# Performance work log

Measured on AMD Instinct MI355X. Metric: run time of the kernel, lower is better.

Reference implementation:

```python
import jax, jax.numpy as jnp
import numpy as np

D_MODEL, N_HEADS, D_K, D_V, D_FF, N_LAYERS = 512, 8, 64, 64, 2048, 6
NEG = -1e9
EPS = 1e-5


def layernorm(x):
    # nn.LayerNorm(d_model) created fresh each call: weight=1, bias=0
    mu = jnp.mean(x, axis=-1, keepdims=True)
    var = jnp.var(x, axis=-1, keepdims=True)
    return (x - mu) * jax.lax.rsqrt(var + EPS)


def sinusoidal_pe(seq_len, d_model, dtype=jnp.float32):
    pos = np.arange(seq_len)[:, None].astype(np.float64)
    div = np.exp(np.arange(0, d_model, 2).astype(np.float64) * (-np.log(10000.0) / d_model))
    pe = np.zeros((seq_len, d_model))
    pe[:, 0::2] = np.sin(pos * div)
    pe[:, 1::2] = np.cos(pos * div)
    return jnp.asarray(pe, dtype=dtype)


def mha(q_in, k_in, v_in, mask, Wq, Wk, Wv, Wo):
    # q_in: [B,Lq,D]; k_in/v_in: [B,Lk,D]; mask: [B,Lq,Lk] bool (True = masked)
    B, Lq, _ = q_in.shape
    Lk = k_in.shape[1]
    Q = (q_in @ Wq).reshape(B, Lq, N_HEADS, D_K).transpose(0, 2, 1, 3)
    K = (k_in @ Wk).reshape(B, Lk, N_HEADS, D_K).transpose(0, 2, 1, 3)
    V = (v_in @ Wv).reshape(B, Lk, N_HEADS, D_V).transpose(0, 2, 1, 3)
    scores = jnp.einsum('bhqd,bhkd->bhqk', Q, K) / jnp.sqrt(jnp.asarray(D_K, q_in.dtype))
    scores = jnp.where(mask[:, None, :, :], jnp.asarray(NEG, scores.dtype), scores)
    attn = jax.nn.softmax(scores, axis=-1)
    ctx = jnp.einsum('bhqk,bhkd->bhqd', attn, V)
    ctx = ctx.transpose(0, 2, 1, 3).reshape(B, Lq, N_HEADS * D_V)
    return layernorm(ctx @ Wo + q_in)


def setup_inputs() -> dict:
    key = jax.random.key(0)
    ks = jax.random.split(key, 16)
    B, T, S, V = 8, 1024, 1024, 32000
    s = 0.02
    inp = {
        'dec_inputs': jax.random.randint(ks[0], (B, T), 0, V),
        'enc_inputs': jax.random.randint(ks[1], (B, S), 0, V),
        'enc_outputs': jax.random.normal(ks[2], (B, S, D_MODEL), jnp.float32),
        'emb': jax.random.normal(ks[3], (V, D_MODEL), jnp.float32) * s,
        'Wq_self': jax.random.normal(ks[4], (N_LAYERS, D_MODEL, N_HEADS * D_K), jnp.float32) * s,
        'Wk_self': jax.random.normal(ks[5], (N_LAYERS, D_MODEL, N_HEADS * D_K), jnp.float32) * s,
        'Wv_self': jax.random.normal(ks[6], (N_LAYERS, D_MODEL, N_HEADS * D_V), jnp.float32) * s,
        'Wo_self': jax.random.normal(ks[7], (N_LAYERS, N_HEADS * D_V, D_MODEL), jnp.float32) * s,
        'Wq_cross': jax.random.normal(ks[8], (N_LAYERS, D_MODEL, N_HEADS * D_K), jnp.float32) * s,
        'Wk_cross': jax.random.normal(ks[9], (N_LAYERS, D_MODEL, N_HEADS * D_K), jnp.float32) * s,
        'Wv_cross': jax.random.normal(ks[10], (N_LAYERS, D_MODEL, N_HEADS * D_V), jnp.float32) * s,
        'Wo_cross': jax.random.normal(ks[11], (N_LAYERS, N_HEADS * D_V, D_MODEL), jnp.float32) * s,
        'W1': jax.random.normal(ks[12], (N_LAYERS, D_MODEL, D_FF), jnp.float32) * s,
        'W2': jax.random.normal(ks[13], (N_LAYERS, D_FF, D_MODEL), jnp.float32) * s,
    }
    return inp


def reference(dec_inputs, enc_inputs, enc_outputs, emb, Wq_self, Wk_self, Wv_self, Wo_self,
              Wq_cross, Wk_cross, Wv_cross, Wo_cross, W1, W2):
    B, T = dec_inputs.shape
    S = enc_inputs.shape[1]
    # embedding with padding_idx=0 (row 0 forced to zero)
    emb_eff = emb.at[0].set(0.0)
    x = emb_eff[dec_inputs] + sinusoidal_pe(T, D_MODEL, emb.dtype)[None, :, :]
    # masks: True = masked
    pad_self = (dec_inputs == 0)[:, None, :]                       # [B,1,T]
    causal = jnp.triu(jnp.ones((T, T), bool), k=1)[None, :, :]     # [1,T,T]
    self_mask = pad_self | causal                                  # [B,T,T]
    enc_mask = jnp.broadcast_to((enc_inputs == 0)[:, None, :], (B, T, S))

    def layer(x, p):
        wqs, wks, wvs, wos, wqc, wkc, wvc, woc, w1, w2 = p
        x = mha(x, x, x, self_mask, wqs, wks, wvs, wos)
        x = mha(x, enc_outputs, enc_outputs, enc_mask, wqc, wkc, wvc, woc)
        h = jax.nn.relu(x @ w1) @ w2
        return layernorm(h + x), None

    params = (Wq_self, Wk_self, Wv_self, Wo_self, Wq_cross, Wk_cross, Wv_cross, Wo_cross, W1, W2)
    x, _ = jax.lax.scan(layer, x, params)
    return x
```

## Files before the change

### kernel.cpp

```cpp
#include <hip/hip_runtime.h>
#include <hip/hip_bf16.h>

#define DMODEL 512
#define NH     8
#define DHEAD  64
#define DFF    2048
#define NLAYER 6
#define BB     8
#define TT     1024
#define NTOK   (BB*TT)
#define ACTE   ((size_t)NTOK*DMODEL)

#define QSCALE 0.18033688011112042f

#define RESCALE_THR 8.0f

typedef __bf16  bf16x8  __attribute__((ext_vector_type(8)));
typedef float   float4v __attribute__((ext_vector_type(4)));
typedef short   short4v __attribute__((ext_vector_type(4)));
typedef short   short8v __attribute__((ext_vector_type(8)));

__device__ __forceinline__ unsigned short f2bf(float f) {
    __hip_bfloat16 h = __float2bfloat16(f);
    return *reinterpret_cast<unsigned short*>(&h);
}

__device__ __forceinline__ void gl_lds16(const void* g, void* l) {
    __builtin_amdgcn_global_load_lds((const __attribute__((address_space(1))) void*)g,
                                     (__attribute__((address_space(3))) void*)l, 16, 0, 0);
}

__device__ __forceinline__ int sigma64(int x) {
    return (x & 32) | ((x & 12) << 1) | ((x & 16) >> 2) | (x & 3);
}

struct Tr8Args {
    const float* src[8];
    unsigned short* dst[8];
    int dstL[8];
    int rowOff[8];
};
__global__ __launch_bounds__(256) void transpose8_kernel(Tr8Args a)
{
    __shared__ float tile[64][65];
    const int type = blockIdx.z / 6, lyr = blockIdx.z % 6;
    const float* src = a.src[type] + (size_t)lyr * 512 * 512;
    unsigned short* dst = a.dst[type] + (size_t)lyr * a.dstL[type];
    const int rowOff = a.rowOff[type];
    const int k0 = blockIdx.x * 64, n0 = blockIdx.y * 64;
    const int tid = threadIdx.x;
#pragma unroll
    for (int rep = 0; rep < 16; ++rep) {
        int idx = rep * 256 + tid;
        int r = idx >> 6, c = idx & 63;
        tile[r][c] = src[(size_t)(k0 + r) * 512 + n0 + c];
    }
    __syncthreads();
#pragma unroll
    for (int rep = 0; rep < 16; ++rep) {
        int idx = rep * 256 + tid;
        int r = idx >> 6, c = idx & 63;
        dst[(size_t)(rowOff + n0 + r) * 512 + k0 + c] = f2bf(tile[c][r]);
    }
}

__global__ __launch_bounds__(256) void transpose_conv_kernel(
    const float* __restrict__ W, unsigned short* __restrict__ Wt, int K, int N,
    size_t dstL, int rowOff)
{
    __shared__ float tile[64][65];
    const float* src = W + (size_t)blockIdx.z * K * N;
    unsigned short* dst = Wt + (size_t)blockIdx.z * dstL;
    const int k0 = blockIdx.x * 64, n0 = blockIdx.y * 64;
    const int tid = threadIdx.x;
#pragma unroll
    for (int rep = 0; rep < 16; ++rep) {
        int idx = rep * 256 + tid;
        int r = idx >> 6, c = idx & 63;
        tile[r][c] = src[(size_t)(k0 + r) * N + n0 + c];
    }
    __syncthreads();
#pragma unroll
    for (int rep = 0; rep < 16; ++rep) {
        int idx = rep * 256 + tid;
        int r = idx >> 6, c = idx & 63;
        dst[(size_t)(rowOff + n0 + r) * K + k0 + c] = f2bf(tile[c][r]);
    }
}

__global__ __launch_bounds__(256) void conv_bf16_kernel(
    const float* __restrict__ in, unsigned short* __restrict__ o)
{
    int i = (blockIdx.x * 256 + threadIdx.x) * 4;
    float4v v = *(const float4v*)(in + i);
    short4v w;
    w[0] = (short)f2bf(v[0]); w[1] = (short)f2bf(v[1]);
    w[2] = (short)f2bf(v[2]); w[3] = (short)f2bf(v[3]);
    *(short4v*)(o + i) = w;
}

__global__ __launch_bounds__(256) void embed_kernel(
    const int* __restrict__ dec, const float* __restrict__ emb,
    unsigned short* __restrict__ xb)
{
    const int row = blockIdx.x;
    const int t = row & (TT - 1);
    const int tid = threadIdx.x;
    const int tok = dec[row];
#pragma unroll
    for (int rep = 0; rep < 2; ++rep) {
        int c = tid + rep * 256;
        float e = (tok != 0) ? emb[(size_t)tok * DMODEL + c] : 0.f;
        int j = c >> 1;
        float freq = __expf(-(float)(2 * j) * (9.210340371976184f / 512.f));
        float ang = (float)t * freq;
        float pe = (c & 1) ? cosf(ang) : sinf(ang);
        xb[(size_t)row * DMODEL + c] = f2bf(e + pe);
    }
}

__global__ __launch_bounds__(256) void add_ln2(
    const float* __restrict__ t, unsigned short* __restrict__ xb,
    float* __restrict__ xout)
{
    const int lane = threadIdx.x & 63;
    const int row = blockIdx.x * 4 + (threadIdx.x >> 6);
    const size_t idx = (size_t)row * DMODEL + lane * 8;
    float4v t0 = *(const float4v*)(t + idx);
    float4v t1 = *(const float4v*)(t + idx + 4);
    float4v u0 = *(const float4v*)(t + ACTE + idx);
    float4v u1 = *(const float4v*)(t + ACTE + idx + 4);
    bf16x8 rb = *(const bf16x8*)(xb + idx);
    float v[8];
#pragma unroll
    for (int k = 0; k < 4; ++k) {
        v[k] = t0[k] + u0[k] + (float)rb[k];
        v[4 + k] = t1[k] + u1[k] + (float)rb[4 + k];
    }
    float s = 0.f, sq = 0.f;
#pragma unroll
    for (int k = 0; k < 8; ++k) { s += v[k]; sq += v[k] * v[k]; }
#pragma unroll
    for (int o = 1; o < 64; o <<= 1) { s += __shfl_xor(s, o); sq += __shfl_xor(sq, o); }
    float mu = s * (1.f / 512.f);
    float var = sq * (1.f / 512.f) - mu * mu;
    float rstd = rsqrtf(var + 1e-5f);
    if (xout) {
        float4v y0, y1;
#pragma unroll
        for (int k = 0; k < 4; ++k) { y0[k] = (v[k] - mu) * rstd; y1[k] = (v[4 + k] - mu) * rstd; }
        *(float4v*)(xout + idx) = y0;
        *(float4v*)(xout + idx + 4) = y1;
    } else {
        short8v w;
#pragma unroll
        for (int k = 0; k < 8; ++k) w[k] = (short)f2bf((v[k] - mu) * rstd);
        *(short8v*)(xb + idx) = w;
    }
}

template <int EPI, int SPLITK = 1>
__global__ __launch_bounds__(256) void gemm_bt(
    const unsigned short* __restrict__ A,
    const unsigned short* __restrict__ Bt,
    float* __restrict__ Cf,
    unsigned short* __restrict__ Cb,
    int M, int N, int K)
{
    __shared__ __attribute__((aligned(16))) short As[128 * 32];
    __shared__ __attribute__((aligned(16))) short Bs[128 * 32];
    const int tid = threadIdx.x;
    const int lane = tid & 63, wv = tid >> 6;
    const int quad = lane >> 4, l15 = lane & 15;
    const int m0 = blockIdx.x * 128, n0 = blockIdx.y * 128;
    const int wm = wv & 1, wn = wv >> 1;

    float4v acc[4][4];
#pragma unroll
    for (int i = 0; i < 4; ++i)
#pragma unroll
        for (int j = 0; j < 4; ++j) acc[i][j] = (float4v){0.f, 0.f, 0.f, 0.f};

    const int Kc = K / SPLITK;
    const int kbeg = (SPLITK > 1) ? (int)blockIdx.z * Kc : 0;
    for (int k0 = kbeg; k0 < kbeg + Kc; k0 += 32) {
#pragma unroll
        for (int i = 0; i < 2; ++i) {
            const int inst = wv * 2 + i;
            const int row = inst * 16 + (lane >> 2);
            const int cb = (lane & 3) ^ ((row >> 1) & 3);
            gl_lds16(A + (size_t)(m0 + row) * K + k0 + cb * 8, (char*)As + inst * 1024);
            gl_lds16(Bt + (size_t)(n0 + row) * K + k0 + cb * 8, (char*)Bs + inst * 1024);
        }
        __syncthreads();
        bf16x8 a[4], b[4];
#pragma unroll
        for (int i = 0; i < 4; ++i) {
            const int r = wm * 64 + i * 16 + l15;
            const int st = quad ^ ((r >> 1) & 3);
            a[i] = *(const bf16x8*)&As[r * 32 + st * 8];
        }
#pragma unroll
        for (int j = 0; j < 4; ++j) {
            const int r = wn * 64 + j * 16 + l15;
            const int st = quad ^ ((r >> 1) & 3);
            b[j] = *(const bf16x8*)&Bs[r * 32 + st * 8];
        }
#pragma unroll
        for (int i = 0; i < 4; ++i)
#pragma unroll
            for (int j = 0; j < 4; ++j)
                acc[i][j] = __builtin_amdgcn_mfma_f32_16x16x32_bf16(a[i], b[j], acc[i][j], 0, 0, 0);
        __syncthreads();
    }

    const size_t zoff = (SPLITK > 1) ? (size_t)blockIdx.z * ACTE : 0;
#pragma unroll
    for (int i = 0; i < 4; ++i) {
        const int row_base = m0 + wm * 64 + i * 16 + quad * 4;
#pragma unroll
        for (int j = 0; j < 4; ++j) {
            const int col = n0 + wn * 64 + j * 16 + l15;
#pragma unroll
            for (int r = 0; r < 4; ++r) {
                const int row = row_base + r;
                const float v = acc[i][j][r];
                if (EPI == 0) {
                    Cf[zoff + (size_t)row * N + col] = v;
                } else if (EPI == 1) {
                    Cb[(size_t)row * N + col] = f2bf(fmaxf(v, 0.f));
                } else if (EPI == 2) {
                    const int which = col >> 9;
                    const float sc = (which == 0) ? QSCALE : 1.f;
                    const int b_ = row >> 10, t = row & (TT - 1);
                    const int h = (col >> 6) & 7, d = col & 63;
                    Cb[(size_t)which * ACTE + (((size_t)(b_ * NH + h)) * TT + t) * DHEAD + d] = f2bf(v * sc);
                } else {
                    const int layer = col >> 10, which = (col >> 9) & 1;
                    const int b_ = row >> 10, t = row & (TT - 1);
                    const int h = (col >> 6) & 7, d = col & 63;
                    Cb[(size_t)(layer * 2 + which) * ACTE +
                       (((size_t)(b_ * NH + h)) * TT + t) * DHEAD + d] = f2bf(v);
                }
            }
        }
    }
}

template <bool CAUSAL>
__global__ __launch_bounds__(256, 4) void attn_kernel(
    const unsigned short* __restrict__ Q,
    const unsigned short* __restrict__ Kb,
    const unsigned short* __restrict__ Vb,
    const int* __restrict__ tokens,
    unsigned short* __restrict__ ctx)
{
    __shared__ __attribute__((aligned(16))) short Ks[2][64 * 64];
    __shared__ __attribute__((aligned(16))) short Vt[2][64 * 64];

    const int tid = threadIdx.x, lane = tid & 63, wv = tid >> 6;
    const int quad = lane >> 4, l15 = lane & 15;
    const int bh = blockIdx.x;
    const int qt = CAUSAL ? (15 - (int)blockIdx.y) : (int)blockIdx.y;
    const int b = bh >> 3, h = bh & 7;
    const size_t kvbase = (size_t)bh * TT * DHEAD;

    const int qcol = wv * 16 + l15;
    const int qg = qt * 64 + qcol;

    const bf16x8 qa0 = *(const bf16x8*)&Q[kvbase + (size_t)qg * DHEAD + quad * 8];
    const bf16x8 qa1 = *(const bf16x8*)&Q[kvbase + (size_t)qg * DHEAD + 32 + quad * 8];

    float4v O[4];
#pragma unroll
    for (int j = 0; j < 4; ++j) O[j] = (float4v){0.f, 0.f, 0.f, 0.f};
    float m_ = -INFINITY, l_ = 0.f;

    const int sig = sigma64(lane);

    const int key0 = (lane & 31) * 2;
    const int d0 = (lane >> 5) * 8 + wv * 16;
    auto stageK = [&](int kt_, int buf) {
#pragma unroll
        for (int i = 0; i < 2; ++i) {
            const int inst = wv * 2 + i;
            const int row = inst * 8 + (lane >> 3);
            const int cb = (lane & 7) ^ (row & 7);
            gl_lds16(Kb + kvbase + (size_t)(kt_ * 64 + sigma64(row)) * DHEAD + cb * 8,
                     (char*)Ks[buf] + inst * 1024);
        }
    };
    auto loadV = [&](int kt_, short8v& r0, short8v& r1) {
        const unsigned short* vp = Vb + kvbase + (size_t)(kt_ * 64 + key0) * DHEAD + d0;
        r0 = *(const short8v*)vp;
        r1 = *(const short8v*)(vp + DHEAD);
    };
    auto writeV = [&](int buf, const short8v& r0, const short8v& r1) {
        const int kc = key0 >> 3, ko = key0 & 7;
#pragma unroll
        for (int j = 0; j < 8; ++j) {
            const int d = d0 + j;
            unsigned pk = (unsigned)(unsigned short)r0[j] |
                          ((unsigned)(unsigned short)r1[j] << 16);
            *(unsigned*)&Vt[buf][d * 64 + ((kc ^ (d & 7)) << 3) + ko] = pk;
        }
    };

    const int nkt = CAUSAL ? (qt + 1) : 16;

    stageK(0, 0);
    {
        short8v v0a, v0b;
        loadV(0, v0a, v0b);
        writeV(0, v0a, v0b);
    }
    int tok_cur = tokens[(size_t)b * TT + sig];
    __syncthreads();

    short8v vn0, vn1;
    int tok_next = 0;
    for (int kt = 0; kt < nkt; ++kt) {
        const int cur = kt & 1, nxt = cur ^ 1;
        const bool more = (kt + 1 < nkt);
        if (more) {
            stageK(kt + 1, nxt);
            loadV(kt + 1, vn0, vn1);
            tok_next = tokens[(size_t)b * TT + (kt + 1) * 64 + sig];
        }
        const unsigned long long kbits = __ballot(tok_cur == 0);

        float4v st[4];
        __builtin_amdgcn_s_setprio(1);
#pragma unroll
        for (int i = 0; i < 4; ++i) {
            const int row = i * 16 + l15;
            const int x = row & 7;
            const bf16x8 k0 = *(const bf16x8*)&Ks[cur][row * 64 + ((quad ^ x)) * 8];
            const bf16x8 k1 = *(const bf16x8*)&Ks[cur][row * 64 + (((4 + quad) ^ x)) * 8];
            float4v z = (float4v){0.f, 0.f, 0.f, 0.f};
            z = __builtin_amdgcn_mfma_f32_16x16x32_bf16(k0, qa0, z, 0, 0, 0);
            z = __builtin_amdgcn_mfma_f32_16x16x32_bf16(k1, qa1, z, 0, 0, 0);
            st[i] = z;
        }
        __builtin_amdgcn_s_setprio(0);

        const bool diag = CAUSAL && (kt == qt);
        const bool domask = (kbits != 0ull) || diag;
        float sv[16], smax = -INFINITY;
        if (domask) {
#pragma unroll
            for (int i = 0; i < 4; ++i)
#pragma unroll
                for (int r = 0; r < 4; ++r) {
                    const int kl = i * 16 + quad * 4 + r;
                    const int klocal = sigma64(kl);
                    const bool mk = ((kbits >> kl) & 1ull) || (diag && klocal > qcol);
                    const float s = mk ? -1e9f : st[i][r];
                    sv[i * 4 + r] = s;
                    smax = fmaxf(smax, s);
                }
        } else {
#pragma unroll
            for (int i = 0; i < 4; ++i)
#pragma unroll
                for (int r = 0; r < 4; ++r) {
                    const float s = st[i][r];
                    sv[i * 4 + r] = s;
                    smax = fmaxf(smax, s);
                }
        }
        smax = fmaxf(smax, __shfl_xor(smax, 16));
        smax = fmaxf(smax, __shfl_xor(smax, 32));
        const bool resc = !__all(smax - m_ <= RESCALE_THR);
        const float mnew = resc ? fmaxf(m_, smax) : m_;
        float tsum = 0.f;
#pragma unroll
        for (int i = 0; i < 16; ++i) {
            float pv = __builtin_amdgcn_exp2f(sv[i] - mnew);
            sv[i] = pv; tsum += pv;
        }
        tsum += __shfl_xor(tsum, 16);
        tsum += __shfl_xor(tsum, 32);

        short8v pw0, pw1;
#pragma unroll
        for (int t = 0; t < 8; ++t) {
            pw0[t] = (short)f2bf(sv[t]);
            pw1[t] = (short)f2bf(sv[8 + t]);
        }
        const bf16x8 p0 = *reinterpret_cast<const bf16x8*>(&pw0);
        const bf16x8 p1 = *reinterpret_cast<const bf16x8*>(&pw1);

        if (resc) {
            const float alpha = __builtin_amdgcn_exp2f(m_ - mnew);
            l_ = l_ * alpha + tsum;
            m_ = mnew;
            float4v av;
#pragma unroll
            for (int r = 0; r < 4; ++r) av[r] = __shfl(alpha, quad * 4 + r);
#pragma unroll
            for (int j = 0; j < 4; ++j) O[j] = O[j] * av;
        } else {
            l_ += tsum;
        }

        __builtin_amdgcn_s_setprio(1);
#pragma unroll
        for (int j = 0; j < 4; ++j) {
            const int row = j * 16 + l15;
            const int x = row & 7;
            const bf16x8 v0 = *(const bf16x8*)&Vt[cur][row * 64 + ((quad ^ x)) * 8];
            const bf16x8 v1 = *(const bf16x8*)&Vt[cur][row * 64 + (((4 + quad) ^ x)) * 8];
            float4v o = O[j];
            o = __builtin_amdgcn_mfma_f32_16x16x32_bf16(p0, v0, o, 0, 0, 0);
            o = __builtin_amdgcn_mfma_f32_16x16x32_bf16(p1, v1, o, 0, 0, 0);
            O[j] = o;
        }
        __builtin_amdgcn_s_setprio(0);

        if (more) {
            writeV(nxt, vn0, vn1);
            tok_cur = tok_next;
        }
        __syncthreads();
    }

    {
        float4v lw;
#pragma unroll
        for (int r = 0; r < 4; ++r) lw[r] = __shfl(l_, quad * 4 + r);
        float rl[4];
#pragma unroll
        for (int r = 0; r < 4; ++r) rl[r] = __builtin_amdgcn_rcpf(lw[r]);
#pragma unroll
        for (int j = 0; j < 4; ++j)
#pragma unroll
            for (int r = 0; r < 4; ++r) {
                const int qrow = qt * 64 + wv * 16 + quad * 4 + r;
                ctx[((size_t)b * TT + qrow) * DMODEL + h * DHEAD + j * 16 + l15] =
                    f2bf(O[j][r] * rl[r]);
            }
    }
}

extern "C" void kernel_launch(void* const* d_in, const int* in_sizes, int n_in,
                              void* d_out, int out_size, void* d_ws, size_t ws_size,
                              hipStream_t stream)
{
    const int* dec = (const int*)d_in[0];
    const int* enc = (const int*)d_in[1];
    const float* enc_out = (const float*)d_in[2];
    const float* emb = (const float*)d_in[3];
    const float* Wq_s = (const float*)d_in[4];
    const float* Wk_s = (const float*)d_in[5];
    const float* Wv_s = (const float*)d_in[6];
    const float* Wo_s = (const float*)d_in[7];
    const float* Wq_c = (const float*)d_in[8];
    const float* Wk_c = (const float*)d_in[9];
    const float* Wv_c = (const float*)d_in[10];
    const float* Wo_c = (const float*)d_in[11];
    const float* W1 = (const float*)d_in[12];
    const float* W2 = (const float*)d_in[13];
    float* out = (float*)d_out;

    char* p = (char*)d_ws;
    auto carve = [&](size_t bytes) -> char* {
        char* r = p;
        p += (bytes + 255) & ~(size_t)255;
        return r;
    };
    unsigned short* xb   = (unsigned short*)carve(ACTE * 2);
    float* tmp1          = (float*)carve(2 * ACTE * 4);
    unsigned short* qkvb = (unsigned short*)carve(3 * ACTE * 2);
    unsigned short* ctxb = (unsigned short*)carve(ACTE * 2);
    unsigned short* encb = (unsigned short*)carve(ACTE * 2);
    unsigned short* h1   = (unsigned short*)carve((size_t)NTOK * DFF * 2);
    unsigned short* wqkvT = (unsigned short*)carve((size_t)NLAYER * 1536 * 512 * 2);
    unsigned short* woT   = (unsigned short*)carve((size_t)NLAYER * 512 * 512 * 2);
    unsigned short* wqcT  = (unsigned short*)carve((size_t)NLAYER * 512 * 512 * 2);
    unsigned short* wkvcT = (unsigned short*)carve((size_t)NLAYER * 1024 * 512 * 2);
    unsigned short* wocT  = (unsigned short*)carve((size_t)NLAYER * 512 * 512 * 2);
    unsigned short* w1T   = (unsigned short*)carve((size_t)NLAYER * 2048 * 512 * 2);
    unsigned short* w2T   = (unsigned short*)carve((size_t)NLAYER * 512 * 2048 * 2);
    const size_t used = (size_t)(p - (char*)d_ws);
    const bool pre = (used + 12 * ACTE * 2 + 256) <= ws_size;
    unsigned short* KVc = pre ? (unsigned short*)carve(12 * ACTE * 2) : nullptr;

    Tr8Args ta;
    ta.src[0] = Wq_s; ta.dst[0] = wqkvT; ta.dstL[0] = 1536 * 512; ta.rowOff[0] = 0;
    ta.src[1] = Wk_s; ta.dst[1] = wqkvT; ta.dstL[1] = 1536 * 512; ta.rowOff[1] = 512;
    ta.src[2] = Wv_s; ta.dst[2] = wqkvT; ta.dstL[2] = 1536 * 512; ta.rowOff[2] = 1024;
    ta.src[3] = Wo_s; ta.dst[3] = woT;   ta.dstL[3] = 512 * 512;  ta.rowOff[3] = 0;
    ta.src[4] = Wq_c; ta.dst[4] = wqcT;  ta.dstL[4] = 512 * 512;  ta.rowOff[4] = 0;
    ta.src[5] = Wk_c; ta.dst[5] = wkvcT; ta.dstL[5] = 1024 * 512; ta.rowOff[5] = 0;
    ta.src[6] = Wv_c; ta.dst[6] = wkvcT; ta.dstL[6] = 1024 * 512; ta.rowOff[6] = 512;
    ta.src[7] = Wo_c; ta.dst[7] = wocT;  ta.dstL[7] = 512 * 512;  ta.rowOff[7] = 0;
    transpose8_kernel<<<dim3(8, 8, 48), 256, 0, stream>>>(ta);
    transpose_conv_kernel<<<dim3(8, 32, NLAYER), 256, 0, stream>>>(W1, w1T, 512, 2048, (size_t)2048 * 512, 0);
    transpose_conv_kernel<<<dim3(32, 8, NLAYER), 256, 0, stream>>>(W2, w2T, 2048, 512, (size_t)512 * 2048, 0);
    conv_bf16_kernel<<<(int)(ACTE / 1024), 256, 0, stream>>>(enc_out, encb);
    embed_kernel<<<NTOK, 256, 0, stream>>>(dec, emb, xb);

    if (pre)
        gemm_bt<3><<<dim3(64, 48), 256, 0, stream>>>(encb, wkvcT, nullptr, KVc, NTOK, 6144, 512);

    for (int lyr = 0; lyr < NLAYER; ++lyr) {
        const unsigned short* wqkv = wqkvT + (size_t)lyr * 1536 * 512;
        const unsigned short* wo   = woT + (size_t)lyr * 512 * 512;
        const unsigned short* wqc  = wqcT + (size_t)lyr * 512 * 512;
        const unsigned short* wkvc = wkvcT + (size_t)lyr * 1024 * 512;
        const unsigned short* woc  = wocT + (size_t)lyr * 512 * 512;
        const unsigned short* w1   = w1T + (size_t)lyr * 2048 * 512;
        const unsigned short* w2   = w2T + (size_t)lyr * 512 * 2048;

        gemm_bt<2><<<dim3(64, 12), 256, 0, stream>>>(xb, wqkv, nullptr, qkvb, NTOK, 1536, 512);
        attn_kernel<true><<<dim3(BB * NH, 16), 256, 0, stream>>>(
            qkvb, qkvb + ACTE, qkvb + 2 * ACTE, dec, ctxb);
        gemm_bt<0, 2><<<dim3(64, 4, 2), 256, 0, stream>>>(ctxb, wo, tmp1, nullptr, NTOK, 512, 512);
        add_ln2<<<NTOK / 4, 256, 0, stream>>>(tmp1, xb, nullptr);

        gemm_bt<2><<<dim3(64, 4), 256, 0, stream>>>(xb, wqc, nullptr, qkvb, NTOK, 512, 512);
        const unsigned short* Kc;
        if (pre) {
            Kc = KVc + (size_t)lyr * 2 * ACTE;
        } else {
            gemm_bt<2><<<dim3(64, 8), 256, 0, stream>>>(encb, wkvc, nullptr, qkvb + ACTE, NTOK, 1024, 512);
            Kc = qkvb + ACTE;
        }
        attn_kernel<false><<<dim3(BB * NH, 16), 256, 0, stream>>>(
            qkvb, Kc, Kc + ACTE, enc, ctxb);
        gemm_bt<0, 2><<<dim3(64, 4, 2), 256, 0, stream>>>(ctxb, woc, tmp1, nullptr, NTOK, 512, 512);
        add_ln2<<<NTOK / 4, 256, 0, stream>>>(tmp1, xb, nullptr);

        gemm_bt<1><<<dim3(64, 16), 256, 0, stream>>>(xb, w1, nullptr, h1, NTOK, 2048, 512);
        gemm_bt<0, 2><<<dim3(64, 4, 2), 256, 0, stream>>>(h1, w2, tmp1, nullptr, NTOK, 512, 2048);
        add_ln2<<<NTOK / 4, 256, 0, stream>>>(tmp1, xb, (lyr == NLAYER - 1) ? out : nullptr);
    }
    (void)in_sizes; (void)n_in; (void)out_size;
}
```

Before: 1.560 ms.

## Process two query tiles per cross-attention block and deepen GEMM K-step to 64

Cross-attention blocks now handle two 64-row query tiles per block, with K/V fragments loaded once from LDS and reused across both softmax chains. This halves the grid and the K/V staging traffic per query, and gives more independent MFMA work to interleave. The cost is higher register pressure, so occupancy is lowered to 2 waves. Separately, the GEMM now stages two 32-wide K chunks per barrier pair, halving syncthreads count at the cost of double the LDS footprint.

```diff
diff --git a/kernel.cpp b/kernel.cpp
--- a/kernel.cpp
+++ b/kernel.cpp
@@ -167,8 +167,8 @@
     unsigned short* __restrict__ Cb,
     int M, int N, int K)
 {
-    __shared__ __attribute__((aligned(16))) short As[128 * 32];
-    __shared__ __attribute__((aligned(16))) short Bs[128 * 32];
+    __shared__ __attribute__((aligned(16))) short As[2 * 128 * 32];
+    __shared__ __attribute__((aligned(16))) short Bs[2 * 128 * 32];
     const int tid = threadIdx.x;
     const int lane = tid & 63, wv = tid >> 6;
     const int quad = lane >> 4, l15 = lane & 15;
@@ -183,34 +183,41 @@
 
     const int Kc = K / SPLITK;
     const int kbeg = (SPLITK > 1) ? (int)blockIdx.z * Kc : 0;
-    for (int k0 = kbeg; k0 < kbeg + Kc; k0 += 32) {
-#pragma unroll
-        for (int i = 0; i < 2; ++i) {
-            const int inst = wv * 2 + i;
-            const int row = inst * 16 + (lane >> 2);
-            const int cb = (lane & 3) ^ ((row >> 1) & 3);
-            gl_lds16(A + (size_t)(m0 + row) * K + k0 + cb * 8, (char*)As + inst * 1024);
-            gl_lds16(Bt + (size_t)(n0 + row) * K + k0 + cb * 8, (char*)Bs + inst * 1024);
-        }
+    for (int k0 = kbeg; k0 < kbeg + Kc; k0 += 64) {
+#pragma unroll
+        for (int c = 0; c < 2; ++c)
+#pragma unroll
+            for (int i = 0; i < 2; ++i) {
+                const int inst = wv * 2 + i;
+                const int row = inst * 16 + (lane >> 2);
+                const int cb = (lane & 3) ^ ((row >> 1) & 3);
+                gl_lds16(A + (size_t)(m0 + row) * K + k0 + c * 32 + cb * 8,
+                         (char*)As + c * 8192 + inst * 1024);
+                gl_lds16(Bt + (size_t)(n0 + row) * K + k0 + c * 32 + cb * 8,
+                         (char*)Bs + c * 8192 + inst * 1024);
+            }
         __syncthreads();
-        bf16x8 a[4], b[4];
-#pragma unroll
-        for (int i = 0; i < 4; ++i) {
-            const int r = wm * 64 + i * 16 + l15;
-            const int st = quad ^ ((r >> 1) & 3);
-            a[i] = *(const bf16x8*)&As[r * 32 + st * 8];
-        }
-#pragma unroll
-        for (int j = 0; j < 4; ++j) {
-            const int r = wn * 64 + j * 16 + l15;
-            const int st = quad ^ ((r >> 1) & 3);
-            b[j] = *(const bf16x8*)&Bs[r * 32 + st * 8];
-        }
-#pragma unroll
-        for (int i = 0; i < 4; ++i)
-#pragma unroll
-            for (int j = 0; j < 4; ++j)
-                acc[i][j] = __builtin_amdgcn_mfma_f32_16x16x32_bf16(a[i], b[j], acc[i][j], 0, 0, 0);
+#pragma unroll
+        for (int c = 0; c < 2; ++c) {
+            bf16x8 a[4], b[4];
+#pragma unroll
+            for (int i = 0; i < 4; ++i) {
+                const int r = wm * 64 + i * 16 + l15;
+                const int st = quad ^ ((r >> 1) & 3);
+                a[i] = *(const bf16x8*)&As[c * 4096 + r * 32 + st * 8];
+            }
+#pragma unroll
+            for (int j = 0; j < 4; ++j) {
+                const int r = wn * 64 + j * 16 + l15;
+                const int st = quad ^ ((r >> 1) & 3);
+                b[j] = *(const bf16x8*)&Bs[c * 4096 + r * 32 + st * 8];
+            }
+#pragma unroll
+            for (int i = 0; i < 4; ++i)
+#pragma unroll
+                for (int j = 0; j < 4; ++j)
+                    acc[i][j] = __builtin_amdgcn_mfma_f32_16x16x32_bf16(a[i], b[j], acc[i][j], 0, 0, 0);
+        }
         __syncthreads();
     }
 
@@ -247,8 +254,8 @@
     }
 }
 
-template <bool CAUSAL>
-__global__ __launch_bounds__(256, 4) void attn_kernel(
+template <bool CAUSAL, int CHAINS>
+__global__ __launch_bounds__(256, (CHAINS == 1 ? 4 : 2)) void attn_kernel(
     const unsigned short* __restrict__ Q,
     const unsigned short* __restrict__ Kb,
     const unsigned short* __restrict__ Vb,
@@ -261,20 +268,27 @@
     const int tid = threadIdx.x, lane = tid & 63, wv = tid >> 6;
     const int quad = lane >> 4, l15 = lane & 15;
     const int bh = blockIdx.x;
-    const int qt = CAUSAL ? (15 - (int)blockIdx.y) : (int)blockIdx.y;
+    const int qt0 = CAUSAL ? (15 - (int)blockIdx.y) : (int)blockIdx.y;
+    const int qt1 = qt0 + 8;
     const int b = bh >> 3, h = bh & 7;
     const size_t kvbase = (size_t)bh * TT * DHEAD;
 
     const int qcol = wv * 16 + l15;
-    const int qg = qt * 64 + qcol;
-
-    const bf16x8 qa0 = *(const bf16x8*)&Q[kvbase + (size_t)qg * DHEAD + quad * 8];
-    const bf16x8 qa1 = *(const bf16x8*)&Q[kvbase + (size_t)qg * DHEAD + 32 + quad * 8];
-
-    float4v O[4];
-#pragma unroll
-    for (int j = 0; j < 4; ++j) O[j] = (float4v){0.f, 0.f, 0.f, 0.f};
-    float m_ = -INFINITY, l_ = 0.f;
+    const int qg0 = qt0 * 64 + qcol;
+    const int qg1 = qt1 * 64 + qcol;
+
+    const bf16x8 qa0 = *(const bf16x8*)&Q[kvbase + (size_t)qg0 * DHEAD + quad * 8];
+    const bf16x8 qa1 = *(const bf16x8*)&Q[kvbase + (size_t)qg0 * DHEAD + 32 + quad * 8];
+    bf16x8 qb0, qb1;
+    if (CHAINS == 2) {
+        qb0 = *(const bf16x8*)&Q[kvbase + (size_t)qg1 * DHEAD + quad * 8];
+        qb1 = *(const bf16x8*)&Q[kvbase + (size_t)qg1 * DHEAD + 32 + quad * 8];
+    }
+
+    float4v O0[4], O1[4];
+#pragma unroll
+    for (int j = 0; j < 4; ++j) { O0[j] = (float4v){0.f,0.f,0.f,0.f}; O1[j] = (float4v){0.f,0.f,0.f,0.f}; }
+    float m0_ = -INFINITY, l0_ = 0.f, m1_ = -INFINITY, l1_ = 0.f;
 
     const int sig = sigma64(lane);
 
@@ -306,7 +320,67 @@
         }
     };
 
-    const int nkt = CAUSAL ? (qt + 1) : 16;
+    auto softmax_step = [&](const float4v* st, unsigned long long kbits, bool diag,
+                            float& m, float& l, float4v* O, bf16x8& p0, bf16x8& p1) {
+        const bool domask = (kbits != 0ull) || diag;
+        float sv[16], smax = -INFINITY;
+        if (domask) {
+#pragma unroll
+            for (int i = 0; i < 4; ++i)
+#pragma unroll
+                for (int r = 0; r < 4; ++r) {
+                    const int kl = i * 16 + quad * 4 + r;
+                    const int klocal = sigma64(kl);
+                    const bool mk = ((kbits >> kl) & 1ull) || (diag && klocal > qcol);
+                    const float s = mk ? -1e9f : st[i][r];
+                    sv[i * 4 + r] = s;
+                    smax = fmaxf(smax, s);
+                }
+        } else {
+#pragma unroll
+            for (int i = 0; i < 4; ++i)
+#pragma unroll
+                for (int r = 0; r < 4; ++r) {
+                    const float s = st[i][r];
+                    sv[i * 4 + r] = s;
+                    smax = fmaxf(smax, s);
+                }
+        }
+        smax = fmaxf(smax, __shfl_xor(smax, 16));
+        smax = fmaxf(smax, __shfl_xor(smax, 32));
+        const bool resc = !__all(smax - m <= RESCALE_THR);
+        const float mnew = resc ? fmaxf(m, smax) : m;
+        float tsum = 0.f;
+#pragma unroll
+        for (int i = 0; i < 16; ++i) {
+            float pv = __builtin_amdgcn_exp2f(sv[i] - mnew);
+            sv[i] = pv; tsum += pv;
+        }
+        tsum += __shfl_xor(tsum, 16);
+        tsum += __shfl_xor(tsum, 32);
+        short8v pw0, pw1;
+#pragma unroll
+        for (int t = 0; t < 8; ++t) {
+            pw0[t] = (short)f2bf(sv[t]);
+            pw1[t] = (short)f2bf(sv[8 + t]);
+        }
+        p0 = *reinterpret_cast<const bf16x8*>(&pw0);
+        p1 = *reinterpret_cast<const bf16x8*>(&pw1);
+        if (resc) {
+            const float alpha = __builtin_amdgcn_exp2f(m - mnew);
+            l = l * alpha + tsum;
+            m = mnew;
+            float4v av;
+#pragma unroll
+            for (int r = 0; r < 4; ++r) av[r] = __shfl(alpha, quad * 4 + r);
+#pragma unroll
+            for (int j = 0; j < 4; ++j) O[j] = O[j] * av;
+        } else {
+            l += tsum;
+        }
+    };
+
+    const int nkt = CAUSAL ? (qt0 + 1) : 16;
 
     stageK(0, 0);
     {
@@ -329,94 +403,77 @@
         }
         const unsigned long long kbits = __ballot(tok_cur == 0);
 
-        float4v st[4];
-        __builtin_amdgcn_s_setprio(1);
-#pragma unroll
-        for (int i = 0; i < 4; ++i) {
-            const int row = i * 16 + l15;
-            const int x = row & 7;
-            const bf16x8 k0 = *(const bf16x8*)&Ks[cur][row * 64 + ((quad ^ x)) * 8];
-            const bf16x8 k1 = *(const bf16x8*)&Ks[cur][row * 64 + (((4 + quad) ^ x)) * 8];
-            float4v z = (float4v){0.f, 0.f, 0.f, 0.f};
-            z = __builtin_amdgcn_mfma_f32_16x16x32_bf16(k0, qa0, z, 0, 0, 0);
-            z = __builtin_amdgcn_mfma_f32_16x16x32_bf16(k1, qa1, z, 0, 0, 0);
-            st[i] = z;
-        }
-        __builtin_amdgcn_s_setprio(0);
-
-        const bool diag = CAUSAL && (kt == qt);
-        const bool domask = (kbits != 0ull) || diag;
-        float sv[16], smax = -INFINITY;
-        if (domask) {
-#pragma unroll
-            for (int i = 0; i < 4; ++i)
-#pragma unroll
-                for (int r = 0; r < 4; ++r) {
-                    const int kl = i * 16 + quad * 4 + r;
-                    const int klocal = sigma64(kl);
-                    const bool mk = ((kbits >> kl) & 1ull) || (diag && klocal > qcol);
-                    const float s = mk ? -1e9f : st[i][r];
-                    sv[i * 4 + r] = s;
-                    smax = fmaxf(smax, s);
+        if (CHAINS == 1) {
+            float4v st[4];
+            __builtin_amdgcn_s_setprio(1);
+#pragma unroll
+            for (int i = 0; i < 4; ++i) {
+                const int row = i * 16 + l15;
+                const int x = row & 7;
+                const bf16x8 k0 = *(const bf16x8*)&Ks[cur][row * 64 + ((quad ^ x)) * 8];
+                const bf16x8 k1 = *(const bf16x8*)&Ks[cur][row * 64 + (((4 + quad) ^ x)) * 8];
+                float4v z = (float4v){0.f, 0.f, 0.f, 0.f};
+                z = __builtin_amdgcn_mfma_f32_16x16x32_bf16(k0, qa0, z, 0, 0, 0);
+                z = __builtin_amdgcn_mfma_f32_16x16x32_bf16(k1, qa1, z, 0, 0, 0);
+                st[i] = z;
+            }
+            __builtin_amdgcn_s_setprio(0);
+            bf16x8 p0, p1;
+            softmax_step(st, kbits, CAUSAL && (kt == qt0), m0_, l0_, O0, p0, p1);
+            __builtin_amdgcn_s_setprio(1);
+#pragma unroll
+            for (int j = 0; j < 4; ++j) {
+                const int row = j * 16 + l15;
+                const int x = row & 7;
+                const bf16x8 v0 = *(const bf16x8*)&Vt[cur][row * 64 + ((quad ^ x)) * 8];
+                const bf16x8 v1 = *(const bf16x8*)&Vt[cur][row * 64 + (((4 + quad) ^ x)) * 8];
+                float4v o = O0[j];
+                o = __builtin_amdgcn_mfma_f32_16x16x32_bf16(p0, v0, o, 0, 0, 0);
+                o = __builtin_amdgcn_mfma_f32_16x16x32_bf16(p1, v1, o, 0, 0, 0);
+                O0[j] = o;
+            }
+            __builtin_amdgcn_s_setprio(0);
+        } else {
+            bf16x8 kf[4][2], vf[4][2];
+#pragma unroll
+            for (int i = 0; i < 4; ++i) {
+                const int row = i * 16 + l15;
+                const int x = row & 7;
+                kf[i][0] = *(const bf16x8*)&Ks[cur][row * 64 + ((quad ^ x)) * 8];
+                kf[i][1] = *(const bf16x8*)&Ks[cur][row * 64 + (((4 + quad) ^ x)) * 8];
+                vf[i][0] = *(const bf16x8*)&Vt[cur][row * 64 + ((quad ^ x)) * 8];
+                vf[i][1] = *(const bf16x8*)&Vt[cur][row * 64 + (((4 + quad) ^ x)) * 8];
+            }
+#pragma unroll
+            for (int ch = 0; ch < 2; ++ch) {
+                const bf16x8& qf0 = ch ? qb0 : qa0;
+                const bf16x8& qf1 = ch ? qb1 : qa1;
+                float& m = ch ? m1_ : m0_;
+                float& l = ch ? l1_ : l0_;
+                float4v* O = ch ? O1 : O0;
+                float4v st[4];
+                __builtin_amdgcn_s_setprio(1);
+#pragma unroll
+                for (int i = 0; i < 4; ++i) {
+                    float4v z = (float4v){0.f, 0.f, 0.f, 0.f};
+                    z = __builtin_amdgcn_mfma_f32_16x16x32_bf16(kf[i][0], qf0, z, 0, 0, 0);
+                    z = __builtin_amdgcn_mfma_f32_16x16x32_bf16(kf[i][1], qf1, z, 0, 0, 0);
+                    st[i] = z;
                 }
-        } else {
-#pragma unroll
-            for (int i = 0; i < 4; ++i)
-#pragma unroll
-                for (int r = 0; r < 4; ++r) {
-                    const float s = st[i][r];
-                    sv[i * 4 + r] = s;
-                    smax = fmaxf(smax, s);
+                __builtin_amdgcn_s_setprio(0);
+                bf16x8 p0, p1;
+                softmax_step(st, kbits, false, m, l, O, p0, p1);
+                __builtin_amdgcn_s_setprio(1);
+#pragma unroll
+                for (int j = 0; j < 4; ++j) {
+                    float4v o = O[j];
+                    o = __builtin_amdgcn_mfma_f32_16x16x32_bf16(p0, vf[j][0], o, 0, 0, 0);
+                    o = __builtin_amdgcn_mfma_f32_16x16x32_bf16(p1, vf[j][1], o, 0, 0, 0);
+                    O[j] = o;
                 }
-        }
-        smax = fmaxf(smax, __shfl_xor(smax, 16));
-        smax = fmaxf(smax, __shfl_xor(smax, 32));
-        const bool resc = !__all(smax - m_ <= RESCALE_THR);
-        const float mnew = resc ? fmaxf(m_, smax) : m_;
-        float tsum = 0.f;
-#pragma unroll
-        for (int i = 0; i < 16; ++i) {
-            float pv = __builtin_amdgcn_exp2f(sv[i] - mnew);
-            sv[i] = pv; tsum += pv;
-        }
-        tsum += __shfl_xor(tsum, 16);
-        tsum += __shfl_xor(tsum, 32);
-
-        short8v pw0, pw1;
-#pragma unroll
-        for (int t = 0; t < 8; ++t) {
-            pw0[t] = (short)f2bf(sv[t]);
-            pw1[t] = (short)f2bf(sv[8 + t]);
-        }
-        const bf16x8 p0 = *reinterpret_cast<const bf16x8*>(&pw0);
-        const bf16x8 p1 = *reinterpret_cast<const bf16x8*>(&pw1);
-
-        if (resc) {
-            const float alpha = __builtin_amdgcn_exp2f(m_ - mnew);
-            l_ = l_ * alpha + tsum;
-            m_ = mnew;
-            float4v av;
-#pragma unroll
-            for (int r = 0; r < 4; ++r) av[r] = __shfl(alpha, quad * 4 + r);
-#pragma unroll
-            for (int j = 0; j < 4; ++j) O[j] = O[j] * av;
-        } else {
-            l_ += tsum;
-        }
-
-        __builtin_amdgcn_s_setprio(1);
-#pragma unroll
-        for (int j = 0; j < 4; ++j) {
-            const int row = j * 16 + l15;
-            const int x = row & 7;
-            const bf16x8 v0 = *(const bf16x8*)&Vt[cur][row * 64 + ((quad ^ x)) * 8];
-            const bf16x8 v1 = *(const bf16x8*)&Vt[cur][row * 64 + (((4 + quad) ^ x)) * 8];
-            float4v o = O[j];
-            o = __builtin_amdgcn_mfma_f32_16x16x32_bf16(p0, v0, o, 0, 0, 0);
-            o = __builtin_amdgcn_mfma_f32_16x16x32_bf16(p1, v1, o, 0, 0, 0);
-            O[j] = o;
-        }
-        __builtin_amdgcn_s_setprio(0);
+                __builtin_amdgcn_s_setprio(0);
+            }
+        }
 
         if (more) {
             writeV(nxt, vn0, vn1);
@@ -425,10 +482,10 @@
         __syncthreads();
     }
 
-    {
+    auto finalize = [&](float l, float4v* O, int qt) {
         float4v lw;
 #pragma unroll
-        for (int r = 0; r < 4; ++r) lw[r] = __shfl(l_, quad * 4 + r);
+        for (int r = 0; r < 4; ++r) lw[r] = __shfl(l, quad * 4 + r);
         float rl[4];
 #pragma unroll
         for (int r = 0; r < 4; ++r) rl[r] = __builtin_amdgcn_rcpf(lw[r]);
@@ -440,7 +497,9 @@
                 ctx[((size_t)b * TT + qrow) * DMODEL + h * DHEAD + j * 16 + l15] =
                     f2bf(O[j][r] * rl[r]);
             }
-    }
+    };
+    finalize(l0_, O0, qt0);
+    if (CHAINS == 2) finalize(l1_, O1, qt1);
 }
 
 extern "C" void kernel_launch(void* const* d_in, const int* in_sizes, int n_in,
@@ -514,7 +573,7 @@
         const unsigned short* w2   = w2T + (size_t)lyr * 512 * 2048;
 
         gemm_bt<2><<<dim3(64, 12), 256, 0, stream>>>(xb, wqkv, nullptr, qkvb, NTOK, 1536, 512);
-        attn_kernel<true><<<dim3(BB * NH, 16), 256, 0, stream>>>(
+        attn_kernel<true, 1><<<dim3(BB * NH, 16), 256, 0, stream>>>(
             qkvb, qkvb + ACTE, qkvb + 2 * ACTE, dec, ctxb);
         gemm_bt<0, 2><<<dim3(64, 4, 2), 256, 0, stream>>>(ctxb, wo, tmp1, nullptr, NTOK, 512, 512);
         add_ln2<<<NTOK / 4, 256, 0, stream>>>(tmp1, xb, nullptr);
@@ -527,7 +586,7 @@
             gemm_bt<2><<<dim3(64, 8), 256, 0, stream>>>(encb, wkvc, nullptr, qkvb + ACTE, NTOK, 1024, 512);
             Kc = qkvb + ACTE;
         }
-        attn_kernel<false><<<dim3(BB * NH, 16), 256, 0, stream>>>(
+        attn_kernel<false, 2><<<dim3(BB * NH, 8), 256, 0, stream>>>(
             qkvb, Kc, Kc + ACTE, enc, ctxb);
         gemm_bt<0, 2><<<dim3(64, 4, 2), 256, 0, stream>>>(ctxb, woc, tmp1, nullptr, NTOK, 512, 512);
         add_ln2<<<NTOK / 4, 256, 0, stream>>>(tmp1, xb, nullptr);
```

Result: faster. 1.475 ms (-5.4%).
